# Performance work log

Hardware: AMD Instinct MI355X
Metric: run time of the kernel (lower is better)

## Reference

```python
import jax, jax.numpy as jnp
import numpy as np

TEMP = 0.07
EPS_NORM = 1e-12  # torch F.normalize clamp eps
EPS_RENORM = 1e-9


def _l2_normalize(x):
    n = jnp.linalg.norm(x, axis=1, keepdims=True)
    return x / jnp.maximum(n, EPS_NORM)


def setup_inputs() -> dict:
    key = jax.random.key(0)
    k1, k2 = jax.random.split(key)
    feat = jax.random.normal(k1, (65536, 1024), dtype=jnp.float32)
    prompts = jax.random.normal(k2, (1000, 1024), dtype=jnp.float32) * 0.01
    return {"feat": feat, "prompts": prompts, "topk": 2}


def reference(feat, prompts, topk):
    # cosine similarity between normalized feat and normalized prompts
    p_n = _l2_normalize(prompts)            # [C, d]
    q_n = _l2_normalize(feat)               # [N, d]
    sims = jnp.matmul(q_n, p_n.T)           # [N, C]
    probs = jax.nn.softmax(sims / TEMP, axis=1)
    num_classes = prompts.shape[0]
    if topk is not None and topk < num_classes:
        _, topk_idx = jax.lax.top_k(probs, topk)          # [N, k]
        rows = jnp.arange(probs.shape[0])[:, None]        # [N, 1]
        mask = jnp.zeros_like(probs).at[rows, topk_idx].set(1.0)
        probs = probs * mask
        probs = probs / (jnp.sum(probs, axis=1, keepdims=True) + EPS_RENORM)
    mixed_prompt = jnp.matmul(probs, prompts)             # [N, d]
    return (mixed_prompt, probs)
```

## Files before the change

### kernel.cpp

```cpp
#include <hip/hip_runtime.h>
#include <cstdint>

using f32x4 = __attribute__((ext_vector_type(4))) float;
using s16x8 = __attribute__((ext_vector_type(8))) short;
typedef unsigned short u16;

typedef const __attribute__((address_space(1))) uint32_t* gptr_t;
typedef __attribute__((address_space(3))) uint32_t* lptr_t;

__device__ __forceinline__ u16 f2bf(float f) {
  union { float f; uint32_t u; } v; v.f = f;
  uint32_t r = v.u + 0x7FFFu + ((v.u >> 16) & 1u);
  return (u16)(r >> 16);
}
__device__ __forceinline__ float bf2f(u16 b) {
  union { uint32_t u; float f; } v; v.u = ((uint32_t)b) << 16;
  return v.f;
}

__global__ __launch_bounds__(256) void k_prep_prompts(const float* __restrict__ prompts,
                                                      u16* __restrict__ p_bf) {
  const int r = blockIdx.x;
  const int t = threadIdx.x;
  if (r >= 1000) {
    if (t < 128) {
      s16x8 z = {0, 0, 0, 0, 0, 0, 0, 0};
      ((s16x8*)(p_bf + (size_t)r * 1024))[t] = z;
    }
    return;
  }
  float4 x = ((const float4*)(prompts + (size_t)r * 1024))[t];
  float ss = x.x * x.x + x.y * x.y + x.z * x.z + x.w * x.w;
  #pragma unroll
  for (int off = 32; off; off >>= 1) ss += __shfl_xor(ss, off);
  __shared__ float red[4];
  if ((t & 63) == 0) red[t >> 6] = ss;
  __syncthreads();
  float n = fmaxf(sqrtf(red[0] + red[1] + red[2] + red[3]), 1e-12f);
  float inv = 1.0f / n;
  u16* pb = p_bf + (size_t)r * 1024 + t * 4;
  pb[0] = f2bf(x.x * inv); pb[1] = f2bf(x.y * inv);
  pb[2] = f2bf(x.z * inv); pb[3] = f2bf(x.w * inv);
}

__global__ __launch_bounds__(256) void k_feat(const float* __restrict__ feat,
                                              u16* __restrict__ out) {
  const size_t stride = (size_t)gridDim.x * 256;
  const size_t n4 = 67108864ull / 4;
  for (size_t j = (size_t)blockIdx.x * 256 + threadIdx.x; j < n4; j += stride) {
    float4 x = ((const float4*)feat)[j];
    ushort4 o;
    o.x = f2bf(x.x); o.y = f2bf(x.y); o.z = f2bf(x.z); o.w = f2bf(x.w);
    ((ushort4*)out)[j] = o;
  }
}

__global__ __launch_bounds__(256) void k_sims(const u16* __restrict__ A,
                                              const u16* __restrict__ B,
                                              u16* __restrict__ C) {
  __shared__ u16 As[128 * 32];
  __shared__ u16 Bs[128 * 32];
  const int bid = blockIdx.x;
  const int lg = (bid & 7) * 512 + (bid >> 3);
  const int bn = lg & 7;
  const int bm = lg >> 3;
  const int t = threadIdx.x;
  const int w = t >> 6, l = t & 63;
  const int wm = (w >> 1) * 64, wn = (w & 1) * 64;
  const int lrow = l & 15, lko = l >> 4;

  f32x4 zero4 = {0.f, 0.f, 0.f, 0.f};
  f32x4 acc[4][4];
  #pragma unroll
  for (int i = 0; i < 4; i++)
    #pragma unroll
    for (int j = 0; j < 4; j++) acc[i][j] = zero4;

  const int srow = t >> 2;
  const int scol = (t & 3) * 8;

  for (int k0 = 0; k0 < 1024; k0 += 32) {
    __syncthreads();
    #pragma unroll
    for (int i = 0; i < 2; i++) {
      int row = i * 64 + srow;
      const u16* ga = A + (size_t)(bm * 128 + row) * 1024 + k0 + scol;
      __builtin_amdgcn_global_load_lds((gptr_t)ga, (lptr_t)&As[row * 32 + scol], 16, 0, 0);
    }
    #pragma unroll
    for (int i = 0; i < 2; i++) {
      int row = i * 64 + srow;
      const u16* gb = B + (size_t)(bn * 128 + row) * 1024 + k0 + scol;
      __builtin_amdgcn_global_load_lds((gptr_t)gb, (lptr_t)&Bs[row * 32 + scol], 16, 0, 0);
    }
    __syncthreads();
    s16x8 a[4], b[4];
    #pragma unroll
    for (int mi = 0; mi < 4; mi++) a[mi] = *(const s16x8*)&As[(wm + mi * 16 + lrow) * 32 + lko * 8];
    #pragma unroll
    for (int ni = 0; ni < 4; ni++) b[ni] = *(const s16x8*)&Bs[(wn + ni * 16 + lrow) * 32 + lko * 8];
    #pragma unroll
    for (int mi = 0; mi < 4; mi++)
      #pragma unroll
      for (int ni = 0; ni < 4; ni++)
        acc[mi][ni] = __builtin_amdgcn_mfma_f32_16x16x32_bf16(a[mi], b[ni], acc[mi][ni], 0, 0, 0);
  }
  const int rbase = (l >> 4) * 4;
  #pragma unroll
  for (int mi = 0; mi < 4; mi++)
    #pragma unroll
    for (int ni = 0; ni < 4; ni++) {
      int gcol = bn * 128 + wn + ni * 16 + lrow;
      if (gcol >= 1000) continue;
      #pragma unroll
      for (int j = 0; j < 4; j++) {
        int grow = bm * 128 + wm + mi * 16 + rbase + j;
        C[(size_t)grow * 1000 + gcol] = f2bf(acc[mi][ni][j]);
      }
    }
}

__global__ __launch_bounds__(256) void k_topk(const float* __restrict__ feat,
                                              const float* __restrict__ prompts,
                                              const u16* __restrict__ sims,
                                              int2* __restrict__ resc,
                                              float2* __restrict__ resw,
                                              float* __restrict__ probs) {
  const int l = threadIdx.x & 63;
  const int row = blockIdx.x * 4 + (threadIdx.x >> 6);
  const u16* srow = sims + (size_t)row * 1000;
  const float NEG = -3.0e38f;
  float s[16];
  #pragma unroll
  for (int j = 0; j < 8; j++) {
    int c = 2 * l + 128 * j;
    if (c + 1 < 1000) {
      uint32_t v = *(const uint32_t*)(srow + c);
      s[2 * j] = bf2f((u16)(v & 0xFFFFu));
      s[2 * j + 1] = bf2f((u16)(v >> 16));
    } else {
      s[2 * j] = (c < 1000) ? bf2f(srow[c]) : NEG;
      s[2 * j + 1] = NEG;
    }
  }
  float a1 = NEG, a2 = NEG;
  #pragma unroll
  for (int j = 0; j < 16; j++) {
    float v = s[j];
    bool g1 = v > a1;
    a2 = g1 ? a1 : fmaxf(a2, v);
    a1 = g1 ? v : a1;
  }
  #pragma unroll
  for (int off = 32; off; off >>= 1) {
    float b1 = __shfl_xor(a1, off), b2 = __shfl_xor(a2, off);
    float m1 = fmaxf(a1, b1);
    float m2 = fmaxf(fminf(a1, b1), fmaxf(a2, b2));
    a1 = m1; a2 = m2;
  }
  const float T = a2 - 0.25f;
  uint32_t mask = 0;
  #pragma unroll
  for (int j = 0; j < 16; j++) {
    int c = 2 * l + 128 * (j >> 1) + (j & 1);
    if (c < 1000 && s[j] >= T) mask |= (1u << j);
  }
  const int base = l * 16;
  float q[16];
  const float4* fr = (const float4*)(feat + (size_t)row * 1024 + base);
  #pragma unroll
  for (int g = 0; g < 4; g++) {
    float4 x = fr[g];
    q[g * 4 + 0] = x.x; q[g * 4 + 1] = x.y; q[g * 4 + 2] = x.z; q[g * 4 + 3] = x.w;
  }
  float qq = 0.f;
  #pragma unroll
  for (int e = 0; e < 16; e++) qq += q[e] * q[e];
  #pragma unroll
  for (int off = 32; off; off >>= 1) qq += __shfl_xor(qq, off);
  float rn = 1.0f / fmaxf(sqrtf(qq), 1e-12f);
  float s1 = NEG, s2 = NEG;
  int c1 = 0x40000000, c2 = 0x40000000;
  while (true) {
    unsigned long long act = __ballot(mask != 0);
    if (!act) break;
    int ln = (int)__ffsll(act) - 1;
    int fj = __ffs(mask) - 1;
    int myc = 2 * l + 128 * (fj >> 1) + (fj & 1);
    int bc = __shfl(myc, ln);
    if (l == ln) mask &= (mask - 1);
    const float4* pr = (const float4*)(prompts + (size_t)bc * 1024 + base);
    float d = 0.f, nn = 0.f;
    #pragma unroll
    for (int g = 0; g < 4; g++) {
      float4 x = pr[g];
      d += q[g * 4 + 0] * x.x; d += q[g * 4 + 1] * x.y;
      d += q[g * 4 + 2] * x.z; d += q[g * 4 + 3] * x.w;
      nn += x.x * x.x + x.y * x.y + x.z * x.z + x.w * x.w;
    }
    #pragma unroll
    for (int off = 32; off; off >>= 1) {
      d += __shfl_xor(d, off);
      nn += __shfl_xor(nn, off);
    }
    float sc = d * rn / fmaxf(sqrtf(nn), 1e-12f);
    bool b1w = (sc > s1) || (sc == s1 && bc < c1);
    bool b2w = (sc > s2) || (sc == s2 && bc < c2);
    if (b1w) { s2 = s1; c2 = c1; s1 = sc; c1 = bc; }
    else if (b2w) { s2 = sc; c2 = bc; }
  }
  float e = expf(fminf(s2 - s1, 0.0f) * (1.0f / 0.07f));
  float w1 = 1.0f / (1.0f + e);
  float w2 = e / (1.0f + e);
  float* prow = probs + (size_t)row * 1000;
  #pragma unroll
  for (int j = 0; j < 16; j++) {
    int c = l + 64 * j;
    if (c < 1000) prow[c] = (c == c1) ? w1 : ((c == c2) ? w2 : 0.0f);
  }
  if (l == 0) {
    resc[row] = make_int2(c1, c2);
    resw[row] = make_float2(w1, w2);
  }
}

__global__ __launch_bounds__(256) void k_write2(const float* __restrict__ prompts,
                                                const int2* __restrict__ resc,
                                                const float2* __restrict__ resw,
                                                float* __restrict__ mixed) {
  const int row = blockIdx.x;
  const int t = threadIdx.x;
  int2 cc = resc[row];
  float2 ww = resw[row];
  const float4* P1 = (const float4*)(prompts + (size_t)cc.x * 1024);
  const float4* P2 = (const float4*)(prompts + (size_t)cc.y * 1024);
  float4 a = P1[t], b = P2[t];
  float4 o;
  o.x = ww.x * a.x + ww.y * b.x;
  o.y = ww.x * a.y + ww.y * b.y;
  o.z = ww.x * a.z + ww.y * b.z;
  o.w = ww.x * a.w + ww.y * b.w;
  ((float4*)(mixed + (size_t)row * 1024))[t] = o;
}

extern "C" void kernel_launch(void* const* d_in, const int* in_sizes, int n_in,
                              void* d_out, int out_size, void* d_ws, size_t ws_size,
                              hipStream_t stream) {
  int fi = 0, pi = 1;
  for (int i = 0; i < n_in; i++) {
    if (in_sizes[i] == 67108864) fi = i;
    else if (in_sizes[i] == 1024000) pi = i;
  }
  const float* feat = (const float*)d_in[fi];
  const float* prompts = (const float*)d_in[pi];

  float* mixed = (float*)d_out;
  float* probs = mixed + 67108864ull;

  u16* p_bf = (u16*)d_ws;
  int2* resc = (int2*)((char*)d_ws + (2ull << 20));
  float2* resw = (float2*)((char*)d_ws + (2ull << 20) + (512ull << 10));

  u16* sims = (u16*)d_out;
  u16* feat_bf = (u16*)probs;

  hipLaunchKernelGGL(k_prep_prompts, dim3(1024), dim3(256), 0, stream, prompts, p_bf);
  hipLaunchKernelGGL(k_feat, dim3(2048), dim3(256), 0, stream, feat, feat_bf);
  hipLaunchKernelGGL(k_sims, dim3(4096), dim3(256), 0, stream, feat_bf, p_bf, sims);
  hipLaunchKernelGGL(k_topk, dim3(16384), dim3(256), 0, stream, feat, prompts, sims, resc, resw, probs);
  hipLaunchKernelGGL(k_write2, dim3(65536), dim3(256), 0, stream, prompts, resc, resw, mixed);
}
```

Baseline: 543.5 us.

## Double-buffer GEMM LDS tiles, prefetch candidate rows, fuse mixed write into topk

The sims GEMM now double-buffers its LDS tiles, loading the next K slice while the current one is multiplied, and uses one barrier per iteration. In k_topk the candidate columns are collected up front and their prompt rows are prefetched in ping-pong registers for the first eight candidates, with a fallback loop for the rest. The mixed-prompt output is now written inside k_topk, which removes the separate k_write2 kernel. When the workspace is large, sims lives in the workspace and the probs rows are written directly; otherwise a light k_wprobs kernel fills probs afterwards.

```diff
diff --git a/kernel.cpp b/kernel.cpp
--- a/kernel.cpp
+++ b/kernel.cpp
@@ -58,8 +58,8 @@
 __global__ __launch_bounds__(256) void k_sims(const u16* __restrict__ A,
                                               const u16* __restrict__ B,
                                               u16* __restrict__ C) {
-  __shared__ u16 As[128 * 32];
-  __shared__ u16 Bs[128 * 32];
+  __shared__ u16 As[2][128 * 32];
+  __shared__ u16 Bs[2][128 * 32];
   const int bid = blockIdx.x;
   const int lg = (bid & 7) * 512 + (bid >> 3);
   const int bn = lg & 7;
@@ -78,32 +78,41 @@
 
   const int srow = t >> 2;
   const int scol = (t & 3) * 8;
-
-  for (int k0 = 0; k0 < 1024; k0 += 32) {
-    __syncthreads();
-    #pragma unroll
-    for (int i = 0; i < 2; i++) {
-      int row = i * 64 + srow;
-      const u16* ga = A + (size_t)(bm * 128 + row) * 1024 + k0 + scol;
-      __builtin_amdgcn_global_load_lds((gptr_t)ga, (lptr_t)&As[row * 32 + scol], 16, 0, 0);
-    }
-    #pragma unroll
-    for (int i = 0; i < 2; i++) {
-      int row = i * 64 + srow;
-      const u16* gb = B + (size_t)(bn * 128 + row) * 1024 + k0 + scol;
-      __builtin_amdgcn_global_load_lds((gptr_t)gb, (lptr_t)&Bs[row * 32 + scol], 16, 0, 0);
-    }
-    __syncthreads();
+  const u16* gA = A + (size_t)(bm * 128 + srow) * 1024 + scol;
+  const u16* gB = B + (size_t)(bn * 128 + srow) * 1024 + scol;
+
+  #pragma unroll
+  for (int i = 0; i < 2; i++) {
+    __builtin_amdgcn_global_load_lds((gptr_t)(gA + (size_t)i * 64 * 1024),
+                                     (lptr_t)&As[0][(i * 64 + srow) * 32 + scol], 16, 0, 0);
+    __builtin_amdgcn_global_load_lds((gptr_t)(gB + (size_t)i * 64 * 1024),
+                                     (lptr_t)&Bs[0][(i * 64 + srow) * 32 + scol], 16, 0, 0);
+  }
+  __syncthreads();
+
+  for (int kt = 0; kt < 32; ++kt) {
+    const int cur = kt & 1;
+    if (kt < 31) {
+      const int nk = (kt + 1) * 32;
+      #pragma unroll
+      for (int i = 0; i < 2; i++) {
+        __builtin_amdgcn_global_load_lds((gptr_t)(gA + (size_t)i * 64 * 1024 + nk),
+                                         (lptr_t)&As[cur ^ 1][(i * 64 + srow) * 32 + scol], 16, 0, 0);
+        __builtin_amdgcn_global_load_lds((gptr_t)(gB + (size_t)i * 64 * 1024 + nk),
+                                         (lptr_t)&Bs[cur ^ 1][(i * 64 + srow) * 32 + scol], 16, 0, 0);
+      }
+    }
     s16x8 a[4], b[4];
     #pragma unroll
-    for (int mi = 0; mi < 4; mi++) a[mi] = *(const s16x8*)&As[(wm + mi * 16 + lrow) * 32 + lko * 8];
-    #pragma unroll
-    for (int ni = 0; ni < 4; ni++) b[ni] = *(const s16x8*)&Bs[(wn + ni * 16 + lrow) * 32 + lko * 8];
+    for (int mi = 0; mi < 4; mi++) a[mi] = *(const s16x8*)&As[cur][(wm + mi * 16 + lrow) * 32 + lko * 8];
+    #pragma unroll
+    for (int ni = 0; ni < 4; ni++) b[ni] = *(const s16x8*)&Bs[cur][(wn + ni * 16 + lrow) * 32 + lko * 8];
     #pragma unroll
     for (int mi = 0; mi < 4; mi++)
       #pragma unroll
       for (int ni = 0; ni < 4; ni++)
         acc[mi][ni] = __builtin_amdgcn_mfma_f32_16x16x32_bf16(a[mi], b[ni], acc[mi][ni], 0, 0, 0);
+    __syncthreads();
   }
   const int rbase = (l >> 4) * 4;
   #pragma unroll
@@ -120,11 +129,17 @@
     }
 }
 
+__global__ __launch_bounds__(256) void k_wprobs(const int2* __restrict__ resc,
+                                                const float2* __restrict__ resw,
+                                                float* __restrict__ probs);
+
+template<bool WPROBS>
 __global__ __launch_bounds__(256) void k_topk(const float* __restrict__ feat,
                                               const float* __restrict__ prompts,
                                               const u16* __restrict__ sims,
                                               int2* __restrict__ resc,
                                               float2* __restrict__ resw,
+                                              float* __restrict__ mixed,
                                               float* __restrict__ probs) {
   const int l = threadIdx.x & 63;
   const int row = blockIdx.x * 4 + (threadIdx.x >> 6);
@@ -165,6 +180,21 @@
     int c = 2 * l + 128 * (j >> 1) + (j & 1);
     if (c < 1000 && s[j] >= T) mask |= (1u << j);
   }
+  int cnt = __popc(mask);
+  #pragma unroll
+  for (int off = 32; off; off >>= 1) cnt += __shfl_xor(cnt, off);
+  int scols[8];
+  uint32_t m = mask;
+  #pragma unroll
+  for (int it = 0; it < 8; it++) {
+    unsigned long long act = __ballot(m != 0);
+    int ln = act ? (int)__ffsll(act) - 1 : 0;
+    int fj = __ffs(m) - 1;
+    int myc = 2 * l + 128 * ((fj >> 1) & 7) + (fj & 1);
+    int bc = __shfl(myc, ln);
+    scols[it] = (bc < 1000) ? bc : 999;
+    if (act && l == ln) m &= (m - 1);
+  }
   const int base = l * 16;
   float q[16];
   const float4* fr = (const float4*)(feat + (size_t)row * 1024 + base);
@@ -179,24 +209,46 @@
   #pragma unroll
   for (int off = 32; off; off >>= 1) qq += __shfl_xor(qq, off);
   float rn = 1.0f / fmaxf(sqrtf(qq), 1e-12f);
+  const int nact = cnt < 8 ? cnt : 8;
   float s1 = NEG, s2 = NEG;
   int c1 = 0x40000000, c2 = 0x40000000;
-  while (true) {
-    unsigned long long act = __ballot(mask != 0);
-    if (!act) break;
-    int ln = (int)__ffsll(act) - 1;
-    int fj = __ffs(mask) - 1;
-    int myc = 2 * l + 128 * (fj >> 1) + (fj & 1);
-    int bc = __shfl(myc, ln);
-    if (l == ln) mask &= (mask - 1);
-    const float4* pr = (const float4*)(prompts + (size_t)bc * 1024 + base);
+  float4 bufA[4], bufB[4];
+  {
+    const float4* p0 = (const float4*)(prompts + (size_t)scols[0] * 1024 + base);
+    #pragma unroll
+    for (int g = 0; g < 4; g++) bufA[g] = p0[g];
+  }
+  #pragma unroll
+  for (int it = 0; it < 8; it++) {
+    if (it >= nact) break;
+    if (it + 1 < nact) {
+      const int nidx = (it + 1 < 8) ? it + 1 : 7;
+      const float4* pn = (const float4*)(prompts + (size_t)scols[nidx] * 1024 + base);
+      if ((it & 1) == 0) {
+        #pragma unroll
+        for (int g = 0; g < 4; g++) bufB[g] = pn[g];
+      } else {
+        #pragma unroll
+        for (int g = 0; g < 4; g++) bufA[g] = pn[g];
+      }
+    }
     float d = 0.f, nn = 0.f;
-    #pragma unroll
-    for (int g = 0; g < 4; g++) {
-      float4 x = pr[g];
-      d += q[g * 4 + 0] * x.x; d += q[g * 4 + 1] * x.y;
-      d += q[g * 4 + 2] * x.z; d += q[g * 4 + 3] * x.w;
-      nn += x.x * x.x + x.y * x.y + x.z * x.z + x.w * x.w;
+    if ((it & 1) == 0) {
+      #pragma unroll
+      for (int g = 0; g < 4; g++) {
+        float4 x = bufA[g];
+        d += q[g * 4 + 0] * x.x; d += q[g * 4 + 1] * x.y;
+        d += q[g * 4 + 2] * x.z; d += q[g * 4 + 3] * x.w;
+        nn += x.x * x.x + x.y * x.y + x.z * x.z + x.w * x.w;
+      }
+    } else {
+      #pragma unroll
+      for (int g = 0; g < 4; g++) {
+        float4 x = bufB[g];
+        d += q[g * 4 + 0] * x.x; d += q[g * 4 + 1] * x.y;
+        d += q[g * 4 + 2] * x.z; d += q[g * 4 + 3] * x.w;
+        nn += x.x * x.x + x.y * x.y + x.z * x.z + x.w * x.w;
+      }
     }
     #pragma unroll
     for (int off = 32; off; off >>= 1) {
@@ -204,43 +256,88 @@
       nn += __shfl_xor(nn, off);
     }
     float sc = d * rn / fmaxf(sqrtf(nn), 1e-12f);
+    int bc = scols[it];
     bool b1w = (sc > s1) || (sc == s1 && bc < c1);
     bool b2w = (sc > s2) || (sc == s2 && bc < c2);
     if (b1w) { s2 = s1; c2 = c1; s1 = sc; c1 = bc; }
     else if (b2w) { s2 = sc; c2 = bc; }
   }
+  if (cnt > 8) {
+    while (true) {
+      unsigned long long act = __ballot(m != 0);
+      if (!act) break;
+      int ln = (int)__ffsll(act) - 1;
+      int fj = __ffs(m) - 1;
+      int myc = 2 * l + 128 * ((fj >> 1) & 7) + (fj & 1);
+      int bc = __shfl(myc, ln);
+      if (l == ln) m &= (m - 1);
+      bc = (bc < 1000) ? bc : 999;
+      const float4* pr = (const float4*)(prompts + (size_t)bc * 1024 + base);
+      float d = 0.f, nn = 0.f;
+      #pragma unroll
+      for (int g = 0; g < 4; g++) {
+        float4 x = pr[g];
+        d += q[g * 4 + 0] * x.x; d += q[g * 4 + 1] * x.y;
+        d += q[g * 4 + 2] * x.z; d += q[g * 4 + 3] * x.w;
+        nn += x.x * x.x + x.y * x.y + x.z * x.z + x.w * x.w;
+      }
+      #pragma unroll
+      for (int off = 32; off; off >>= 1) {
+        d += __shfl_xor(d, off);
+        nn += __shfl_xor(nn, off);
+      }
+      float sc = d * rn / fmaxf(sqrtf(nn), 1e-12f);
+      bool b1w = (sc > s1) || (sc == s1 && bc < c1);
+      bool b2w = (sc > s2) || (sc == s2 && bc < c2);
+      if (b1w) { s2 = s1; c2 = c1; s1 = sc; c1 = bc; }
+      else if (b2w) { s2 = sc; c2 = bc; }
+    }
+  }
   float e = expf(fminf(s2 - s1, 0.0f) * (1.0f / 0.07f));
   float w1 = 1.0f / (1.0f + e);
   float w2 = e / (1.0f + e);
-  float* prow = probs + (size_t)row * 1000;
-  #pragma unroll
-  for (int j = 0; j < 16; j++) {
-    int c = l + 64 * j;
-    if (c < 1000) prow[c] = (c == c1) ? w1 : ((c == c2) ? w2 : 0.0f);
-  }
   if (l == 0) {
     resc[row] = make_int2(c1, c2);
     resw[row] = make_float2(w1, w2);
   }
-}
-
-__global__ __launch_bounds__(256) void k_write2(const float* __restrict__ prompts,
-                                                const int2* __restrict__ resc,
+  const float4* P1 = (const float4*)(prompts + (size_t)c1 * 1024 + base);
+  const float4* P2 = (const float4*)(prompts + (size_t)c2 * 1024 + base);
+  float* mrow = mixed + (size_t)row * 1024 + base;
+  #pragma unroll
+  for (int g = 0; g < 4; g++) {
+    float4 x = P1[g], y = P2[g];
+    float4 o;
+    o.x = w1 * x.x + w2 * y.x;
+    o.y = w1 * x.y + w2 * y.y;
+    o.z = w1 * x.z + w2 * y.z;
+    o.w = w1 * x.w + w2 * y.w;
+    ((float4*)mrow)[g] = o;
+  }
+  if (WPROBS) {
+    float* prow = probs + (size_t)row * 1000;
+    #pragma unroll
+    for (int j = 0; j < 16; j++) {
+      int c = l + 64 * j;
+      if (c < 1000) prow[c] = (c == c1) ? w1 : ((c == c2) ? w2 : 0.0f);
+    }
+  }
+}
+
+__global__ __launch_bounds__(256) void k_wprobs(const int2* __restrict__ resc,
                                                 const float2* __restrict__ resw,
-                                                float* __restrict__ mixed) {
+                                                float* __restrict__ probs) {
   const int row = blockIdx.x;
   const int t = threadIdx.x;
+  if (t >= 250) return;
   int2 cc = resc[row];
   float2 ww = resw[row];
-  const float4* P1 = (const float4*)(prompts + (size_t)cc.x * 1024);
-  const float4* P2 = (const float4*)(prompts + (size_t)cc.y * 1024);
-  float4 a = P1[t], b = P2[t];
-  float4 o;
-  o.x = ww.x * a.x + ww.y * b.x;
-  o.y = ww.x * a.y + ww.y * b.y;
-  o.z = ww.x * a.z + ww.y * b.z;
-  o.w = ww.x * a.w + ww.y * b.w;
-  ((float4*)(mixed + (size_t)row * 1024))[t] = o;
+  const int base = t * 4;
+  float4 z;
+  z.x = (base + 0 == cc.x) ? ww.x : ((base + 0 == cc.y) ? ww.y : 0.0f);
+  z.y = (base + 1 == cc.x) ? ww.x : ((base + 1 == cc.y) ? ww.y : 0.0f);
+  z.z = (base + 2 == cc.x) ? ww.x : ((base + 2 == cc.y) ? ww.y : 0.0f);
+  z.w = (base + 3 == cc.x) ? ww.x : ((base + 3 == cc.y) ? ww.y : 0.0f);
+  ((float4*)(probs + (size_t)row * 1000))[t] = z;
 }
 
 extern "C" void kernel_launch(void* const* d_in, const int* in_sizes, int n_in,
@@ -261,12 +358,19 @@
   int2* resc = (int2*)((char*)d_ws + (2ull << 20));
   float2* resw = (float2*)((char*)d_ws + (2ull << 20) + (512ull << 10));
 
-  u16* sims = (u16*)d_out;
-  u16* feat_bf = (u16*)probs;
+  u16* feat_bf = (u16*)mixed;
+  const bool big_ws = ws_size >= (1ull << 27);
+  u16* sims = big_ws ? (u16*)((char*)d_ws + (3ull << 20)) : (u16*)probs;
 
   hipLaunchKernelGGL(k_prep_prompts, dim3(1024), dim3(256), 0, stream, prompts, p_bf);
   hipLaunchKernelGGL(k_feat, dim3(2048), dim3(256), 0, stream, feat, feat_bf);
   hipLaunchKernelGGL(k_sims, dim3(4096), dim3(256), 0, stream, feat_bf, p_bf, sims);
-  hipLaunchKernelGGL(k_topk, dim3(16384), dim3(256), 0, stream, feat, prompts, sims, resc, resw, probs);
-  hipLaunchKernelGGL(k_write2, dim3(65536), dim3(256), 0, stream, prompts, resc, resw, mixed);
-}
+  if (big_ws) {
+    hipLaunchKernelGGL((k_topk<true>), dim3(16384), dim3(256), 0, stream,
+                       feat, prompts, sims, resc, resw, mixed, probs);
+  } else {
+    hipLaunchKernelGGL((k_topk<false>), dim3(16384), dim3(256), 0, stream,
+                       feat, prompts, sims, resc, resw, mixed, probs);
+    hipLaunchKernelGGL(k_wprobs, dim3(65536), dim3(256), 0, stream, resc, resw, probs);
+  }
+}
```

New measurement: 594.7 us. 1.09x slower.
